# Kernel tuning notes

Measured on AMD Instinct MI355X. Metric: run time of the kernel, lower is better.

Reference implementation:

```python
import jax, jax.numpy as jnp
import numpy as np

CH = 64
INNER = CH // 2  # 32
EPS = 1e-3  # keras BatchNormalization default epsilon


def setup_inputs() -> dict:
    key = jax.random.key(0)
    ks = jax.random.split(key, 10)
    B, H, W = 4, 64, 64
    s = 0.02
    return {
        "x": jax.random.normal(ks[0], (B, H, W, CH), dtype=jnp.float32),
        "g_W": jax.random.normal(ks[1], (CH, INNER), dtype=jnp.float32) * s,
        "g_b": jnp.zeros((INNER,), dtype=jnp.float32),
        "phi_W": jax.random.normal(ks[2], (CH, INNER), dtype=jnp.float32) * s,
        "phi_b": jnp.zeros((INNER,), dtype=jnp.float32),
        "theta_W": jax.random.normal(ks[3], (CH, INNER), dtype=jnp.float32) * s,
        "theta_b": jnp.zeros((INNER,), dtype=jnp.float32),
        "w_W": jax.random.normal(ks[4], (INNER, CH), dtype=jnp.float32) * s,
        "w_b": jnp.zeros((CH,), dtype=jnp.float32),
        "gamma": jnp.ones((CH,), dtype=jnp.float32),
        "beta": jnp.zeros((CH,), dtype=jnp.float32),
    }


def reference(x, g_W, g_b, phi_W, phi_b, theta_W, theta_b, w_W, w_b, gamma, beta):
    B, H, W, C = x.shape
    N = H * W
    # 1x1 conv projections == per-pixel channel matmuls
    g_x = (jnp.einsum('bhwc,cd->bhwd', x, g_W) + g_b).reshape(B, N, INNER)
    phi_x = (jnp.einsum('bhwc,cd->bhwd', x, phi_W) + phi_b).reshape(B, N, INNER)
    theta_x = (jnp.einsum('bhwc,cd->bhwd', x, theta_W) + theta_b).reshape(B, N, INNER)
    # full self-attention over spatial positions (no scaling, as in source)
    f = jnp.einsum('bnd,bmd->bnm', theta_x, phi_x)           # [B, N, N]
    f = jax.nn.softmax(f, axis=-1)
    y = jnp.einsum('bnm,bmd->bnd', f, g_x).reshape(B, H, W, INNER)
    w_y = jnp.einsum('bhwd,dc->bhwc', y, w_W) + w_b          # [B, H, W, C]
    # BatchNorm (training-mode batch statistics over B,H,W)
    mean = jnp.mean(w_y, axis=(0, 1, 2))
    var = jnp.var(w_y, axis=(0, 1, 2))
    w_y = gamma * (w_y - mean) * jax.lax.rsqrt(var + EPS) + beta
    return x + w_y
```

## Files before the change

kernel.cpp:

```cpp
#include <hip/hip_runtime.h>
#include <hip/hip_bf16.h>
#include <cstddef>
#include <cstdint>

#define EPSV 1e-3f
#define LOG2E 1.4426950408889634f

using f32x4 = __attribute__((ext_vector_type(4))) float;
using bh8   = __attribute__((ext_vector_type(8))) short;

#if defined(__has_builtin)
#  if __has_builtin(__builtin_amdgcn_exp2f)
#    define EXP2F(v) __builtin_amdgcn_exp2f(v)
#  else
#    define EXP2F(v) exp2f(v)
#  endif
#else
#  define EXP2F(v) exp2f(v)
#endif

union F8 { uint2 v; long long ll; };
union BH { uint32_t u[4]; bh8 v; };

static __device__ __forceinline__ uint32_t cvtpkbf(float lo, float hi) {
    uint32_t r;
    asm("v_cvt_pk_bf16_f32 %0, %1, %2" : "=v"(r) : "v"(lo), "v"(hi));
    return r;
}

__global__ __launch_bounds__(256) void proj_kernel(
    const float* __restrict__ x,
    const float* __restrict__ gW, const float* __restrict__ gbias,
    const float* __restrict__ pW, const float* __restrict__ pbias,
    const float* __restrict__ tW, const float* __restrict__ tbias,
    uint8_t* __restrict__ thetab,
    uint8_t* __restrict__ phib,
    uint8_t* __restrict__ gshuf)
{
    __shared__ __align__(16) __hip_bfloat16 wbuf[96*72];
    __shared__ float lbias[96];
    const int tid = threadIdx.x;
    const int pix0 = blockIdx.x * 32;

    #pragma unroll
    for (int j = 0; j < 8; ++j) {
        int idx = tid + 256*j;
        int c = idx >> 5, ol = idx & 31;
        wbuf[(ol)*72 + c]      = __float2bfloat16(tW[idx]);
        wbuf[(32+ol)*72 + c]   = __float2bfloat16(pW[idx]);
        wbuf[(64+ol)*72 + c]   = __float2bfloat16(gW[idx]);
    }
    if (tid < 32) { lbias[tid] = tbias[tid]; lbias[32+tid] = pbias[tid]; lbias[64+tid] = gbias[tid]; }
    __syncthreads();

    const int wv = tid >> 6;
    const int ln = tid & 63;
    const int h = ln >> 4;
    const int r = ln & 15;
    const int mt = wv & 1;

    BH a0, a1;
    {
        const float* xr = x + (size_t)(pix0 + mt*16 + r)*64 + h*8;
        float4 f0 = *(const float4*)xr;
        float4 f1 = *(const float4*)(xr + 4);
        a0.u[0] = cvtpkbf(f0.x, f0.y); a0.u[1] = cvtpkbf(f0.z, f0.w);
        a0.u[2] = cvtpkbf(f1.x, f1.y); a0.u[3] = cvtpkbf(f1.z, f1.w);
        float4 f2 = *(const float4*)(xr + 32);
        float4 f3 = *(const float4*)(xr + 36);
        a1.u[0] = cvtpkbf(f2.x, f2.y); a1.u[1] = cvtpkbf(f2.z, f2.w);
        a1.u[2] = cvtpkbf(f3.x, f3.y); a1.u[3] = cvtpkbf(f3.z, f3.w);
    }

    const int b = pix0 >> 12;
    const int chunk = (pix0 & 4095) >> 5;
    const size_t cb1024 = (size_t)(b*128 + chunk)*1024;

    for (int T = wv; T < 12; T += 4) {
        const int nt = T >> 1;
        bh8 b0 = *(const bh8*)&wbuf[(nt*16 + r)*72 + h*8];
        bh8 b1 = *(const bh8*)&wbuf[(nt*16 + r)*72 + 32 + h*8];
        f32x4 cc = {0.f, 0.f, 0.f, 0.f};
        cc = __builtin_amdgcn_mfma_f32_16x16x32_bf16(a0.v, b0, cc, 0, 0, 0);
        cc = __builtin_amdgcn_mfma_f32_16x16x32_bf16(a1.v, b1, cc, 0, 0, 0);

        const int o = nt*16 + r;
        const float bias = lbias[o];
        if (o < 32) {
            #pragma unroll
            for (int gi = 0; gi < 4; ++gi) {
                int pl = mt*16 + 4*h + gi;
                float v = (cc[gi] + bias) * LOG2E;
                int pk = __builtin_amdgcn_cvt_pk_fp8_f32(v, v, 0, false);
                thetab[(size_t)(pix0 + pl)*32 + o] = (uint8_t)(pk & 0xFF);
            }
        } else if (o < 64) {
            const int f = o - 32;
            const int fh = f >> 3, fb = f & 7;
            #pragma unroll
            for (int gi = 0; gi < 4; ++gi) {
                int loc = mt*16 + 4*h + gi;
                float v = cc[gi] + bias;
                int pk = __builtin_amdgcn_cvt_pk_fp8_f32(v, v, 0, false);
                phib[cb1024 + (size_t)(fh*16 + (loc & 15))*16 + ((loc & 16) ? 8 : 0) + fb]
                    = (uint8_t)(pk & 0xFF);
            }
        } else {
            const int d = o - 64;
            #pragma unroll
            for (int gi = 0; gi < 4; ++gi) {
                int loc = mt*16 + 4*h + gi;
                int t_ = (loc >> 4) & 1;
                int hh = (loc >> 2) & 3;
                int jj = loc & 3;
                int w_ = 8*hh + jj + 4*t_;
                float v = cc[gi] + bias;
                int pk = __builtin_amdgcn_cvt_pk_fp8_f32(v, v, 0, false);
                gshuf[cb1024 + (size_t)((w_ >> 3)*16 + (d & 15))*16 + ((d & 16) ? 8 : 0) + (w_ & 7)]
                    = (uint8_t)(pk & 0xFF);
            }
        }
    }
}

__global__ __launch_bounds__(1024, 4) void attn_kernel(
    const uint8_t* __restrict__ thetab,
    const uint8_t* __restrict__ phib,
    const uint8_t* __restrict__ gshuf,
    const float* __restrict__ wW, const float* __restrict__ wb,
    float* __restrict__ out, float* __restrict__ stats)
{
    __shared__ float yl[16][32][33];
    __shared__ float lred[16][32];
    __shared__ float lwW[2048];
    __shared__ float lwb[64];
    const int tid  = threadIdx.x;
    const int wave = tid >> 6;
    const int lane = tid & 63;
    const int h = lane >> 4;
    const int r = lane & 15;
    const int blk = blockIdx.x;
    const int b = blk >> 6;
    const int q0 = (blk & 63) * 64;
    const int qh = wave >> 3;
    const int kq = wave & 7;
    const int qbase = q0 + qh*32;
    const size_t base = (size_t)b * 4096;

    #pragma unroll
    for (int j = 0; j < 2; ++j) lwW[tid + 1024*j] = wW[tid + 1024*j];
    if (tid < 64) lwb[tid] = wb[tid];

    F8 qaA, qaB;
    qaA.v = *(const uint2*)(thetab + (base + qbase + r)*32 + h*8);
    qaB.v = *(const uint2*)(thetab + (base + qbase + 16 + r)*32 + h*8);
    const uint8_t* phiB = phib  + (size_t)b*131072;
    const uint8_t* gB   = gshuf + (size_t)b*131072;
    const int loff = (h*16 + r)*16;

    f32x4 y0A = {0,0,0,0}, y1A = {0,0,0,0};
    f32x4 y0B = {0,0,0,0}, y1B = {0,0,0,0};
    float lsA = 0.f, lsB = 0.f;

    const int cbeg = kq * 16;

    auto QKEXP = [&](const uint4& kf, F8& pA_, F8& pB_) {
        F8 ka_, kb_;
        ka_.v.x = kf.x; ka_.v.y = kf.y;
        kb_.v.x = kf.z; kb_.v.y = kf.w;
        f32x4 z = {0,0,0,0};
        f32x4 s0A = __builtin_amdgcn_mfma_f32_16x16x32_fp8_fp8(ka_.ll, qaA.ll, z, 0, 0, 0);
        f32x4 s1A = __builtin_amdgcn_mfma_f32_16x16x32_fp8_fp8(kb_.ll, qaA.ll, z, 0, 0, 0);
        f32x4 s0B = __builtin_amdgcn_mfma_f32_16x16x32_fp8_fp8(ka_.ll, qaB.ll, z, 0, 0, 0);
        f32x4 s1B = __builtin_amdgcn_mfma_f32_16x16x32_fp8_fp8(kb_.ll, qaB.ll, z, 0, 0, 0);

        float pA0 = EXP2F(s0A[0]), pA1 = EXP2F(s0A[1]), pA2 = EXP2F(s0A[2]), pA3 = EXP2F(s0A[3]);
        float pA4 = EXP2F(s1A[0]), pA5 = EXP2F(s1A[1]), pA6 = EXP2F(s1A[2]), pA7 = EXP2F(s1A[3]);
        float pB0 = EXP2F(s0B[0]), pB1 = EXP2F(s0B[1]), pB2 = EXP2F(s0B[2]), pB3 = EXP2F(s0B[3]);
        float pB4 = EXP2F(s1B[0]), pB5 = EXP2F(s1B[1]), pB6 = EXP2F(s1B[2]), pB7 = EXP2F(s1B[3]);
        lsA += ((pA0+pA1)+(pA2+pA3)) + ((pA4+pA5)+(pA6+pA7));
        lsB += ((pB0+pB1)+(pB2+pB3)) + ((pB4+pB5)+(pB6+pB7));

        int lo = __builtin_amdgcn_cvt_pk_fp8_f32(pA0, pA1, 0, false);
        lo     = __builtin_amdgcn_cvt_pk_fp8_f32(pA2, pA3, lo, true);
        int hi = __builtin_amdgcn_cvt_pk_fp8_f32(pA4, pA5, 0, false);
        hi     = __builtin_amdgcn_cvt_pk_fp8_f32(pA6, pA7, hi, true);
        pA_.v.x = (uint32_t)lo; pA_.v.y = (uint32_t)hi;
        lo = __builtin_amdgcn_cvt_pk_fp8_f32(pB0, pB1, 0, false);
        lo = __builtin_amdgcn_cvt_pk_fp8_f32(pB2, pB3, lo, true);
        hi = __builtin_amdgcn_cvt_pk_fp8_f32(pB4, pB5, 0, false);
        hi = __builtin_amdgcn_cvt_pk_fp8_f32(pB6, pB7, hi, true);
        pB_.v.x = (uint32_t)lo; pB_.v.y = (uint32_t)hi;
    };

    auto PV = [&](const F8& pA_, const F8& pB_, const uint4& gf) {
        F8 g0_, g1_;
        g0_.v.x = gf.x; g0_.v.y = gf.y;
        g1_.v.x = gf.z; g1_.v.y = gf.w;
        y0A = __builtin_amdgcn_mfma_f32_16x16x32_fp8_fp8(pA_.ll, g0_.ll, y0A, 0, 0, 0);
        y1A = __builtin_amdgcn_mfma_f32_16x16x32_fp8_fp8(pA_.ll, g1_.ll, y1A, 0, 0, 0);
        y0B = __builtin_amdgcn_mfma_f32_16x16x32_fp8_fp8(pB_.ll, g0_.ll, y0B, 0, 0, 0);
        y1B = __builtin_amdgcn_mfma_f32_16x16x32_fp8_fp8(pB_.ll, g1_.ll, y1B, 0, 0, 0);
    };

    uint4 kC, kN, gP, gC, gN;
    kC = *(const uint4*)(phiB + (size_t)cbeg*1024 + loff);
    gP = *(const uint4*)(gB   + (size_t)cbeg*1024 + loff);
    kN = *(const uint4*)(phiB + (size_t)(cbeg + 1)*1024 + loff);
    gC = *(const uint4*)(gB   + (size_t)(cbeg + 1)*1024 + loff);

    F8 paA0, paB0;
    QKEXP(kC, paA0, paB0);
    kC = kN;

    for (int t = 1; t < 16; ++t) {
        const int nc = (t + 1 < 16) ? cbeg + t + 1 : cbeg;
        kN = *(const uint4*)(phiB + (size_t)nc*1024 + loff);
        gN = *(const uint4*)(gB   + (size_t)nc*1024 + loff);

        PV(paA0, paB0, gP);
        QKEXP(kC, paA0, paB0);

        kC = kN;
        gP = gC; gC = gN;
    }
    PV(paA0, paB0, gP);

    lsA += __shfl_xor(lsA, 16); lsA += __shfl_xor(lsA, 32);
    lsB += __shfl_xor(lsB, 16); lsB += __shfl_xor(lsB, 32);

    #pragma unroll
    for (int gi = 0; gi < 4; ++gi) {
        yl[wave][4*h+gi][r]       = y0A[gi];
        yl[wave][4*h+gi][16+r]    = y1A[gi];
        yl[wave][16+4*h+gi][r]    = y0B[gi];
        yl[wave][16+4*h+gi][16+r] = y1B[gi];
    }
    if (lane < 16) { lred[wave][r] = lsA; lred[wave][16+r] = lsB; }
    __syncthreads();

    {
        const int q   = tid >> 4;
        const int d2  = (tid & 15) * 2;
        const int qh2 = q >> 5;
        const int ql  = q & 31;
        float a0=0.f, a1=0.f, lq=0.f;
        #pragma unroll
        for (int w = 0; w < 8; ++w) {
            a0 += yl[qh2*8+w][ql][d2];
            a1 += yl[qh2*8+w][ql][d2+1];
            lq += lred[qh2*8+w][ql];
        }
        float inv = 1.0f / lq;
        yl[qh2*8][ql][d2]   = a0*inv;
        yl[qh2*8][ql][d2+1] = a1*inv;
    }
    __syncthreads();

    {
        const int p   = lane;
        const int cg_ = wave;
        float acc[4];
        #pragma unroll
        for (int j = 0; j < 4; ++j) acc[j] = lwb[cg_*4 + j];
        for (int d = 0; d < 32; ++d) {
            float yv = yl[(p >> 5)*8][p & 31][d];
            #pragma unroll
            for (int j = 0; j < 4; ++j) acc[j] += yv * lwW[d*64 + cg_*4 + j];
        }
        *(float4*)(out + (size_t)(base + q0 + p)*64 + cg_*4) = *(float4*)&acc[0];

        float s1[4], s2[4];
        #pragma unroll
        for (int j = 0; j < 4; ++j) { s1[j] = acc[j]; s2[j] = acc[j]*acc[j]; }
        #pragma unroll
        for (int m = 1; m <= 32; m <<= 1) {
            #pragma unroll
            for (int j = 0; j < 4; ++j) {
                s1[j] += __shfl_xor(s1[j], m);
                s2[j] += __shfl_xor(s2[j], m);
            }
        }
        if (lane == 0) {
            #pragma unroll
            for (int j = 0; j < 4; ++j) {
                stats[(size_t)(cg_*4 + j)*256 + blk]        = s1[j];
                stats[(size_t)(64 + cg_*4 + j)*256 + blk]   = s2[j];
            }
        }
    }
}

__global__ __launch_bounds__(256) void apply_kernel(
    const float* __restrict__ stats,
    const float* __restrict__ gamma,
    const float* __restrict__ beta,
    const float* __restrict__ x,
    float* __restrict__ out)
{
    __shared__ float sums1[64];
    __shared__ float sums2[64];
    __shared__ __align__(16) float params[128];
    const int tid = threadIdx.x;
    {
        const int c = tid >> 2;
        const int part = tid & 3;
        const float4* st4 = (const float4*)stats;
        float s1 = 0.f, s2 = 0.f;
        #pragma unroll
        for (int j = 0; j < 16; ++j) {
            float4 v = st4[c*64 + part*16 + j];
            s1 += (v.x + v.y) + (v.z + v.w);
        }
        #pragma unroll
        for (int j = 0; j < 16; ++j) {
            float4 v = st4[(64 + c)*64 + part*16 + j];
            s2 += (v.x + v.y) + (v.z + v.w);
        }
        s1 += __shfl_xor(s1, 1); s1 += __shfl_xor(s1, 2);
        s2 += __shfl_xor(s2, 1); s2 += __shfl_xor(s2, 2);
        if (part == 0) { sums1[c] = s1; sums2[c] = s2; }
    }
    __syncthreads();
    if (tid < 64) {
        float mean = sums1[tid] * (1.0f/16384.0f);
        float var  = sums2[tid] * (1.0f/16384.0f) - mean*mean;
        float sc = gamma[tid] * rsqrtf(var + EPSV);
        params[tid]      = sc;
        params[64 + tid] = beta[tid] - mean*sc;
    }
    __syncthreads();

    const float4* x4 = (const float4*)x;
    float4* o4 = (float4*)out;
    #pragma unroll
    for (int j = 0; j < 4; ++j) {
        int i4 = blockIdx.x*1024 + tid + 256*j;
        int cb = (i4 & 15) * 4;
        float4 v  = o4[i4];
        float4 xv = x4[i4];
        float4 sc = *(const float4*)&params[cb];
        float4 sh = *(const float4*)&params[64 + cb];
        float4 rr;
        rr.x = xv.x + sc.x*v.x + sh.x;
        rr.y = xv.y + sc.y*v.y + sh.y;
        rr.z = xv.z + sc.z*v.z + sh.z;
        rr.w = xv.w + sc.w*v.w + sh.w;
        o4[i4] = rr;
    }
}

extern "C" void kernel_launch(void* const* d_in, const int* in_sizes, int n_in,
                              void* d_out, int out_size, void* d_ws, size_t ws_size,
                              hipStream_t stream)
{
    const float* x     = (const float*)d_in[0];
    const float* gW    = (const float*)d_in[1];
    const float* gb    = (const float*)d_in[2];
    const float* pW    = (const float*)d_in[3];
    const float* pb    = (const float*)d_in[4];
    const float* tW    = (const float*)d_in[5];
    const float* tb    = (const float*)d_in[6];
    const float* wW    = (const float*)d_in[7];
    const float* wb    = (const float*)d_in[8];
    const float* gamma = (const float*)d_in[9];
    const float* beta  = (const float*)d_in[10];
    float* out = (float*)d_out;

    char* w = (char*)d_ws;
    uint8_t* thetab = (uint8_t*)(w);
    uint8_t* phib   = (uint8_t*)(w + (1u<<19));
    uint8_t* gshuf  = (uint8_t*)(w + (2u<<19));
    float* stats    = (float*)(w + (3u<<19));

    proj_kernel<<<512, 256, 0, stream>>>(x, gW, gb, pW, pb, tW, tb, thetab, phib, gshuf);
    attn_kernel<<<256, 1024, 0, stream>>>(thetab, phib, gshuf, wW, wb, out, stats);
    apply_kernel<<<256, 256, 0, stream>>>(stats, gamma, beta, x, out);
}
```

Baseline: 33.90 us.

## Stage phi/g chunks through shared memory and shrink LDS with bf16 partials

Each chunk's phi and g tiles are now loaded once per block pair of waves into a shared staging buffer, with one wave group fetching phi and the other fetching g, instead of every wave reading both from global memory. The per-wave partial y accumulators move from fp32 to bf16 in LDS, which cuts shared memory so launch bounds can request 8 blocks per CU. The cost is two block-wide barriers per loop iteration, the loss of the previous software-pipelined QK/PV overlap, and extra rounding of the partial sums.

```diff
diff --git a/kernel.cpp b/kernel.cpp
--- a/kernel.cpp
+++ b/kernel.cpp
@@ -123,14 +123,15 @@
     }
 }
 
-__global__ __launch_bounds__(1024, 4) void attn_kernel(
+__global__ __launch_bounds__(1024, 8) void attn_kernel(
     const uint8_t* __restrict__ thetab,
     const uint8_t* __restrict__ phib,
     const uint8_t* __restrict__ gshuf,
     const float* __restrict__ wW, const float* __restrict__ wb,
     float* __restrict__ out, float* __restrict__ stats)
 {
-    __shared__ float yl[16][32][33];
+    __shared__ __align__(16) uint8_t stage[8][2][1024];
+    __shared__ __hip_bfloat16 yl[16][32][34];
     __shared__ float lred[16][32];
     __shared__ float lwW[2048];
     __shared__ float lwb[64];
@@ -156,85 +157,79 @@
     qaB.v = *(const uint2*)(thetab + (base + qbase + 16 + r)*32 + h*8);
     const uint8_t* phiB = phib  + (size_t)b*131072;
     const uint8_t* gB   = gshuf + (size_t)b*131072;
-    const int loff = (h*16 + r)*16;
+    const int loff = lane*16;
 
     f32x4 y0A = {0,0,0,0}, y1A = {0,0,0,0};
     f32x4 y0B = {0,0,0,0}, y1B = {0,0,0,0};
     float lsA = 0.f, lsB = 0.f;
 
     const int cbeg = kq * 16;
-
-    auto QKEXP = [&](const uint4& kf, F8& pA_, F8& pB_) {
-        F8 ka_, kb_;
+    const uint8_t* gsrc = (qh == 0) ? phiB : gB;
+
+    uint4 sv = *(const uint4*)(gsrc + (size_t)cbeg*1024 + loff);
+    *(uint4*)&stage[kq][qh][loff] = sv;
+    sv = *(const uint4*)(gsrc + (size_t)(cbeg + 1)*1024 + loff);
+    __syncthreads();
+
+    for (int t = 0; t < 16; ++t) {
+        uint4 kf = *(const uint4*)&stage[kq][0][loff];
+        uint4 gf = *(const uint4*)&stage[kq][1][loff];
+        __syncthreads();
+        if (t + 1 < 16) {
+            *(uint4*)&stage[kq][qh][loff] = sv;
+            if (t + 2 < 16)
+                sv = *(const uint4*)(gsrc + (size_t)(cbeg + t + 2)*1024 + loff);
+        }
+        __syncthreads();
+
+        F8 ka_, kb_, g0_, g1_;
         ka_.v.x = kf.x; ka_.v.y = kf.y;
         kb_.v.x = kf.z; kb_.v.y = kf.w;
-        f32x4 z = {0,0,0,0};
-        f32x4 s0A = __builtin_amdgcn_mfma_f32_16x16x32_fp8_fp8(ka_.ll, qaA.ll, z, 0, 0, 0);
-        f32x4 s1A = __builtin_amdgcn_mfma_f32_16x16x32_fp8_fp8(kb_.ll, qaA.ll, z, 0, 0, 0);
-        f32x4 s0B = __builtin_amdgcn_mfma_f32_16x16x32_fp8_fp8(ka_.ll, qaB.ll, z, 0, 0, 0);
-        f32x4 s1B = __builtin_amdgcn_mfma_f32_16x16x32_fp8_fp8(kb_.ll, qaB.ll, z, 0, 0, 0);
-
-        float pA0 = EXP2F(s0A[0]), pA1 = EXP2F(s0A[1]), pA2 = EXP2F(s0A[2]), pA3 = EXP2F(s0A[3]);
-        float pA4 = EXP2F(s1A[0]), pA5 = EXP2F(s1A[1]), pA6 = EXP2F(s1A[2]), pA7 = EXP2F(s1A[3]);
-        float pB0 = EXP2F(s0B[0]), pB1 = EXP2F(s0B[1]), pB2 = EXP2F(s0B[2]), pB3 = EXP2F(s0B[3]);
-        float pB4 = EXP2F(s1B[0]), pB5 = EXP2F(s1B[1]), pB6 = EXP2F(s1B[2]), pB7 = EXP2F(s1B[3]);
-        lsA += ((pA0+pA1)+(pA2+pA3)) + ((pA4+pA5)+(pA6+pA7));
-        lsB += ((pB0+pB1)+(pB2+pB3)) + ((pB4+pB5)+(pB6+pB7));
-
-        int lo = __builtin_amdgcn_cvt_pk_fp8_f32(pA0, pA1, 0, false);
-        lo     = __builtin_amdgcn_cvt_pk_fp8_f32(pA2, pA3, lo, true);
-        int hi = __builtin_amdgcn_cvt_pk_fp8_f32(pA4, pA5, 0, false);
-        hi     = __builtin_amdgcn_cvt_pk_fp8_f32(pA6, pA7, hi, true);
-        pA_.v.x = (uint32_t)lo; pA_.v.y = (uint32_t)hi;
-        lo = __builtin_amdgcn_cvt_pk_fp8_f32(pB0, pB1, 0, false);
-        lo = __builtin_amdgcn_cvt_pk_fp8_f32(pB2, pB3, lo, true);
-        hi = __builtin_amdgcn_cvt_pk_fp8_f32(pB4, pB5, 0, false);
-        hi = __builtin_amdgcn_cvt_pk_fp8_f32(pB6, pB7, hi, true);
-        pB_.v.x = (uint32_t)lo; pB_.v.y = (uint32_t)hi;
-    };
-
-    auto PV = [&](const F8& pA_, const F8& pB_, const uint4& gf) {
-        F8 g0_, g1_;
         g0_.v.x = gf.x; g0_.v.y = gf.y;
         g1_.v.x = gf.z; g1_.v.y = gf.w;
-        y0A = __builtin_amdgcn_mfma_f32_16x16x32_fp8_fp8(pA_.ll, g0_.ll, y0A, 0, 0, 0);
-        y1A = __builtin_amdgcn_mfma_f32_16x16x32_fp8_fp8(pA_.ll, g1_.ll, y1A, 0, 0, 0);
-        y0B = __builtin_amdgcn_mfma_f32_16x16x32_fp8_fp8(pB_.ll, g0_.ll, y0B, 0, 0, 0);
-        y1B = __builtin_amdgcn_mfma_f32_16x16x32_fp8_fp8(pB_.ll, g1_.ll, y1B, 0, 0, 0);
-    };
-
-    uint4 kC, kN, gP, gC, gN;
-    kC = *(const uint4*)(phiB + (size_t)cbeg*1024 + loff);
-    gP = *(const uint4*)(gB   + (size_t)cbeg*1024 + loff);
-    kN = *(const uint4*)(phiB + (size_t)(cbeg + 1)*1024 + loff);
-    gC = *(const uint4*)(gB   + (size_t)(cbeg + 1)*1024 + loff);
-
-    F8 paA0, paB0;
-    QKEXP(kC, paA0, paB0);
-    kC = kN;
-
-    for (int t = 1; t < 16; ++t) {
-        const int nc = (t + 1 < 16) ? cbeg + t + 1 : cbeg;
-        kN = *(const uint4*)(phiB + (size_t)nc*1024 + loff);
-        gN = *(const uint4*)(gB   + (size_t)nc*1024 + loff);
-
-        PV(paA0, paB0, gP);
-        QKEXP(kC, paA0, paB0);
-
-        kC = kN;
-        gP = gC; gC = gN;
-    }
-    PV(paA0, paB0, gP);
+        f32x4 z = {0,0,0,0};
+
+        {
+            f32x4 s0 = __builtin_amdgcn_mfma_f32_16x16x32_fp8_fp8(ka_.ll, qaA.ll, z, 0, 0, 0);
+            f32x4 s1 = __builtin_amdgcn_mfma_f32_16x16x32_fp8_fp8(kb_.ll, qaA.ll, z, 0, 0, 0);
+            float p0 = EXP2F(s0[0]), p1 = EXP2F(s0[1]), p2 = EXP2F(s0[2]), p3 = EXP2F(s0[3]);
+            float p4 = EXP2F(s1[0]), p5 = EXP2F(s1[1]), p6 = EXP2F(s1[2]), p7 = EXP2F(s1[3]);
+            lsA += ((p0+p1)+(p2+p3)) + ((p4+p5)+(p6+p7));
+            F8 pa;
+            int lo = __builtin_amdgcn_cvt_pk_fp8_f32(p0, p1, 0, false);
+            lo     = __builtin_amdgcn_cvt_pk_fp8_f32(p2, p3, lo, true);
+            int hi = __builtin_amdgcn_cvt_pk_fp8_f32(p4, p5, 0, false);
+            hi     = __builtin_amdgcn_cvt_pk_fp8_f32(p6, p7, hi, true);
+            pa.v.x = (uint32_t)lo; pa.v.y = (uint32_t)hi;
+            y0A = __builtin_amdgcn_mfma_f32_16x16x32_fp8_fp8(pa.ll, g0_.ll, y0A, 0, 0, 0);
+            y1A = __builtin_amdgcn_mfma_f32_16x16x32_fp8_fp8(pa.ll, g1_.ll, y1A, 0, 0, 0);
+        }
+        {
+            f32x4 s0 = __builtin_amdgcn_mfma_f32_16x16x32_fp8_fp8(ka_.ll, qaB.ll, z, 0, 0, 0);
+            f32x4 s1 = __builtin_amdgcn_mfma_f32_16x16x32_fp8_fp8(kb_.ll, qaB.ll, z, 0, 0, 0);
+            float p0 = EXP2F(s0[0]), p1 = EXP2F(s0[1]), p2 = EXP2F(s0[2]), p3 = EXP2F(s0[3]);
+            float p4 = EXP2F(s1[0]), p5 = EXP2F(s1[1]), p6 = EXP2F(s1[2]), p7 = EXP2F(s1[3]);
+            lsB += ((p0+p1)+(p2+p3)) + ((p4+p5)+(p6+p7));
+            F8 pa;
+            int lo = __builtin_amdgcn_cvt_pk_fp8_f32(p0, p1, 0, false);
+            lo     = __builtin_amdgcn_cvt_pk_fp8_f32(p2, p3, lo, true);
+            int hi = __builtin_amdgcn_cvt_pk_fp8_f32(p4, p5, 0, false);
+            hi     = __builtin_amdgcn_cvt_pk_fp8_f32(p6, p7, hi, true);
+            pa.v.x = (uint32_t)lo; pa.v.y = (uint32_t)hi;
+            y0B = __builtin_amdgcn_mfma_f32_16x16x32_fp8_fp8(pa.ll, g0_.ll, y0B, 0, 0, 0);
+            y1B = __builtin_amdgcn_mfma_f32_16x16x32_fp8_fp8(pa.ll, g1_.ll, y1B, 0, 0, 0);
+        }
+    }
 
     lsA += __shfl_xor(lsA, 16); lsA += __shfl_xor(lsA, 32);
     lsB += __shfl_xor(lsB, 16); lsB += __shfl_xor(lsB, 32);
 
     #pragma unroll
     for (int gi = 0; gi < 4; ++gi) {
-        yl[wave][4*h+gi][r]       = y0A[gi];
-        yl[wave][4*h+gi][16+r]    = y1A[gi];
-        yl[wave][16+4*h+gi][r]    = y0B[gi];
-        yl[wave][16+4*h+gi][16+r] = y1B[gi];
+        yl[wave][4*h+gi][r]       = __float2bfloat16(y0A[gi]);
+        yl[wave][4*h+gi][16+r]    = __float2bfloat16(y1A[gi]);
+        yl[wave][16+4*h+gi][r]    = __float2bfloat16(y0B[gi]);
+        yl[wave][16+4*h+gi][16+r] = __float2bfloat16(y1B[gi]);
     }
     if (lane < 16) { lred[wave][r] = lsA; lred[wave][16+r] = lsB; }
     __syncthreads();
@@ -247,13 +242,13 @@
         float a0=0.f, a1=0.f, lq=0.f;
         #pragma unroll
         for (int w = 0; w < 8; ++w) {
-            a0 += yl[qh2*8+w][ql][d2];
-            a1 += yl[qh2*8+w][ql][d2+1];
+            a0 += __bfloat162float(yl[qh2*8+w][ql][d2]);
+            a1 += __bfloat162float(yl[qh2*8+w][ql][d2+1]);
             lq += lred[qh2*8+w][ql];
         }
         float inv = 1.0f / lq;
-        yl[qh2*8][ql][d2]   = a0*inv;
-        yl[qh2*8][ql][d2+1] = a1*inv;
+        yl[qh2*8][ql][d2]   = __float2bfloat16(a0*inv);
+        yl[qh2*8][ql][d2+1] = __float2bfloat16(a1*inv);
     }
     __syncthreads();
 
@@ -264,7 +259,7 @@
         #pragma unroll
         for (int j = 0; j < 4; ++j) acc[j] = lwb[cg_*4 + j];
         for (int d = 0; d < 32; ++d) {
-            float yv = yl[(p >> 5)*8][p & 31][d];
+            float yv = __bfloat162float(yl[(p >> 5)*8][p & 31][d]);
             #pragma unroll
             for (int j = 0; j < 4; ++j) acc[j] += yv * lwW[d*64 + cg_*4 + j];
         }
```

New measurement: 36.08 us. 1.06x slower.
